# Kernel optimization log

Hardware: AMD Instinct MI355X
Metric: run time of the kernel (lower is better)

The kernel has to match this reference:

```python
import jax, jax.numpy as jnp
import numpy as np

N, E, G = 20000, 320000, 128
D, H, C, L = 128, 8, 16, 4  # hidden, heads, per-head dim, layers
F_NODE, F_EDGE, T = 9, 3, 10


def _lin_init(key, fan_in, shape):
    return jax.random.normal(key, shape, dtype=jnp.float32) / np.sqrt(fan_in)


def setup_inputs() -> dict:
    key = jax.random.key(0)
    ks = jax.random.split(key, 24)
    inp = {
        "x": jax.random.normal(ks[0], (N, F_NODE), dtype=jnp.float32),
        "edge_index": jax.random.randint(ks[1], (2, E), 0, N),
        "edge_attr": jax.random.normal(ks[2], (E, F_EDGE), dtype=jnp.float32),
        "batch": jnp.sort(jax.random.randint(ks[3], (N,), 0, G)),
        # encoders
        "node_w": _lin_init(ks[4], F_NODE, (F_NODE, D)), "node_b": jnp.zeros((D,), jnp.float32),
        "edge_w": _lin_init(ks[5], F_EDGE, (F_EDGE, D)), "edge_b": jnp.zeros((D,), jnp.float32),
        # per-layer TransformerConv params (stacked over L)
        "Wq": _lin_init(ks[6], D, (L, D, D)), "bq": jnp.zeros((L, D), jnp.float32),
        "Wk": _lin_init(ks[7], D, (L, D, D)), "bk": jnp.zeros((L, D), jnp.float32),
        "Wv": _lin_init(ks[8], D, (L, D, D)), "bv": jnp.zeros((L, D), jnp.float32),
        "We": _lin_init(ks[9], D, (L, D, D)),  # lin_edge (no bias in PyG)
        "Wskip": _lin_init(ks[10], D, (L, D, D)), "bskip": jnp.zeros((L, D), jnp.float32),
        "Wbeta": _lin_init(ks[11], 3 * D, (L, 3 * D)),  # lin_beta (no bias)
        "ln_g": jnp.ones((L, D), jnp.float32), "ln_b": jnp.zeros((L, D), jnp.float32),
        # prediction head
        "h1_w": _lin_init(ks[12], D, (D, D // 2)), "h1_b": jnp.zeros((D // 2,), jnp.float32),
        "h2_w": _lin_init(ks[13], D // 2, (D // 2, T)), "h2_b": jnp.zeros((T,), jnp.float32),
    }
    return inp


def _layer_norm(x, g, b, eps=1e-5):
    mu = jnp.mean(x, -1, keepdims=True)
    var = jnp.mean(jnp.square(x - mu), -1, keepdims=True)
    return (x - mu) * jax.lax.rsqrt(var + eps) * g + b


def _transformer_conv(h, ea, src, dst, Wq, bq, Wk, bk, Wv, bv, We, Wskip, bskip, Wbeta):
    # PyG TransformerConv, concat=True, beta=True, edge_dim=D, eval mode (no dropout)
    q = (h @ Wq + bq)[dst].reshape(E, H, C)           # query at destination i
    k = (h @ Wk + bk)[src].reshape(E, H, C)
    v = (h @ Wv + bv)[src].reshape(E, H, C)
    e = (ea @ We).reshape(E, H, C)
    k = k + e
    alpha = jnp.sum(q * k, -1) / np.sqrt(C)           # [E, H]
    m = jax.ops.segment_max(alpha, dst, num_segments=N)
    alpha = jnp.exp(alpha - m[dst])
    denom = jax.ops.segment_sum(alpha, dst, num_segments=N)
    alpha = alpha / (denom[dst] + 1e-16)
    msg = (v + e) * alpha[..., None]                  # [E, H, C]
    out = jax.ops.segment_sum(msg, dst, num_segments=N).reshape(N, D)
    x_r = h @ Wskip + bskip                           # root/skip transform
    beta = jax.nn.sigmoid(jnp.concatenate([out, x_r, out - x_r], -1) @ Wbeta)  # [N]
    return beta[:, None] * x_r + (1.0 - beta)[:, None] * out


def reference(x, edge_index, edge_attr, batch, node_w, node_b, edge_w, edge_b,
              Wq, bq, Wk, bk, Wv, bv, We, Wskip, bskip, Wbeta, ln_g, ln_b,
              h1_w, h1_b, h2_w, h2_b):
    src, dst = edge_index[0], edge_index[1]
    h = jax.nn.relu(x @ node_w + node_b)              # node encoder + relu
    ea = edge_attr @ edge_w + edge_b                  # edge encoder
    for l in range(L):
        h_res = h
        h = _transformer_conv(h, ea, src, dst, Wq[l], bq[l], Wk[l], bk[l],
                              Wv[l], bv[l], We[l], Wskip[l], bskip[l], Wbeta[l])
        h = _layer_norm(h + h_res, ln_g[l], ln_b[l])
    # global mean pool over graphs
    sums = jax.ops.segment_sum(h, batch, num_segments=G)
    cnt = jax.ops.segment_sum(jnp.ones((N,), h.dtype), batch, num_segments=G)
    pooled = sums / jnp.maximum(cnt, 1.0)[:, None]    # [G, D]
    return jax.nn.relu(pooled @ h1_w + h1_b) @ h2_w + h2_b  # [G, T]
```

## Files before the change

kernel.cpp:

```cpp
#include <hip/hip_runtime.h>
#include <hip/hip_bf16.h>

typedef __hip_bfloat16 bf16;
typedef __attribute__((ext_vector_type(8))) short short8;
typedef __attribute__((ext_vector_type(4))) float f32x4;

#define DEV __device__ __forceinline__

DEV float blo(unsigned u) { return __uint_as_float(u << 16); }
DEV float bhi(unsigned u) { return __uint_as_float(u & 0xffff0000u); }

DEV float waveReduceSum(float v) {
#pragma unroll
    for (int m = 1; m < 64; m <<= 1) v += __shfl_xor(v, m);
    return v;
}

DEV float red8(float v) {
    v += __shfl_xor(v, 8);
    v += __shfl_xor(v, 16);
    v += __shfl_xor(v, 32);
    return v;
}

__global__ __launch_bounds__(256) void pack_w_k(
    const float* __restrict__ Wq, const float* __restrict__ Wk,
    const float* __restrict__ Wv, const float* __restrict__ Ws,
    bf16* __restrict__ outp, int L) {
    int t = blockIdx.x * 256 + threadIdx.x;
    if (t >= 4 * L * 16384) return;
    int p = t & 16383;
    int ls = t >> 14;
    int l = ls >> 2, s = ls & 3;
    int j = p & 7, ln = (p >> 3) & 63, kb = (p >> 9) & 3, nb = p >> 11;
    int k = kb * 32 + (ln >> 4) * 8 + j;
    int n = nb * 16 + (ln & 15);
    const float* W = (s == 0) ? Wq : (s == 1) ? Wk : (s == 2) ? Wv : Ws;
    outp[t] = __float2bfloat16(W[(size_t)l * 16384 + k * 128 + n]);
}

__global__ __launch_bounds__(256) void pack_b_k(
    const float* __restrict__ bq, const float* __restrict__ bk,
    const float* __restrict__ bv, const float* __restrict__ bs,
    float* __restrict__ outp, int L) {
    int t = blockIdx.x * 256 + threadIdx.x;
    if (t >= 4 * L * 128) return;
    int d = t & 127;
    int ls = t >> 7;
    int l = ls >> 2, s = ls & 3;
    const float* B = (s == 0) ? bq : (s == 1) ? bk : (s == 2) ? bv : bs;
    outp[t] = B[l * 128 + d];
}

__global__ __launch_bounds__(256) void edge_mats_k(
    const float* __restrict__ edge_w, const float* __restrict__ edge_b,
    const float* __restrict__ We, float* __restrict__ Me, int L) {
    int t = blockIdx.x * 256 + threadIdx.x;
    if (t >= L * 4 * 128) return;
    int n = t & 127, j = (t >> 7) & 3, l = t >> 9;
    const float* W = We + (size_t)l * 16384;
    const float* row = (j < 3) ? (edge_w + j * 128) : edge_b;
    float acc = 0.f;
    for (int d = 0; d < 128; ++d) acc += row[d] * W[d * 128 + n];
    Me[t] = acc;
}

__global__ __launch_bounds__(256) void hist_k(const int* __restrict__ ei,
                                              int* __restrict__ deg, int E) {
    int e = blockIdx.x * 256 + threadIdx.x;
    if (e >= E) return;
    atomicAdd(&deg[ei[E + e]], 1);
}

__global__ __launch_bounds__(1024) void scan_k(const int* __restrict__ deg,
                                               int* __restrict__ off,
                                               int* __restrict__ cursor, int N, int E) {
    __shared__ int part[1024];
    int t = threadIdx.x;
    int chunk = (N + 1023) >> 10;
    int lo = t * chunk, hi = min(lo + chunk, N);
    int s = 0;
    for (int i = lo; i < hi; ++i) s += deg[i];
    part[t] = s;
    __syncthreads();
    for (int d = 1; d < 1024; d <<= 1) {
        int v = (t >= d) ? part[t - d] : 0;
        __syncthreads();
        part[t] += v;
        __syncthreads();
    }
    int base = (t == 0) ? 0 : part[t - 1];
    for (int i = lo; i < hi; ++i) {
        off[i] = base;
        cursor[i] = base;
        base += deg[i];
    }
    if (t == 1023) off[N] = E;
}

__global__ __launch_bounds__(256) void fill_k(const int* __restrict__ ei,
                                              const float* __restrict__ eattr,
                                              int* __restrict__ cursor,
                                              int* __restrict__ el_src,
                                              float4* __restrict__ ea4, int E) {
    int e = blockIdx.x * 256 + threadIdx.x;
    if (e >= E) return;
    int dst = ei[E + e];
    int pos = atomicAdd(&cursor[dst], 1);
    el_src[pos] = ei[e];
    ea4[pos] = make_float4(eattr[e * 3], eattr[e * 3 + 1], eattr[e * 3 + 2], 0.f);
}

__global__ __launch_bounds__(256) void node_enc_k(
    const float* __restrict__ x, const float* __restrict__ w,
    const float* __restrict__ b, float* __restrict__ h,
    bf16* __restrict__ h_bf, int N) {
    int t = blockIdx.x * 256 + threadIdx.x;
    if (t >= N * 128) return;
    int n = t >> 7, d = t & 127;
    float acc = b[d];
#pragma unroll
    for (int i = 0; i < 9; ++i) acc += x[n * 9 + i] * w[i * 128 + d];
    float r = fmaxf(acc, 0.f);
    h[t] = r;
    h_bf[t] = __float2bfloat16(r);
}

__global__ __launch_bounds__(256) void qkvs_k(
    const bf16* __restrict__ A, const bf16* __restrict__ Wp,
    const float* __restrict__ bp,
    bf16* __restrict__ Q, bf16* __restrict__ kv,
    float* __restrict__ S, int M) {
    int tid = threadIdx.x;
    int l = tid & 63, w = tid >> 6;
    int row0 = blockIdx.x * 64;
    const short* Ab = (const short*)A + (size_t)(row0 + (l & 15)) * 128 + ((l >> 4) * 8);
    short8 a[4][4];
#pragma unroll
    for (int mb = 0; mb < 4; ++mb)
#pragma unroll
        for (int kb = 0; kb < 4; ++kb)
            a[mb][kb] = *(const short8*)(Ab + mb * 16 * 128 + kb * 32);
    int colb = w * 32 + (l & 15);
#pragma unroll
    for (int s = 0; s < 4; ++s) {
        const short* Wb = (const short*)Wp + s * 16384;
        short8 bfr[2][4];
#pragma unroll
        for (int nbi = 0; nbi < 2; ++nbi)
#pragma unroll
            for (int kb = 0; kb < 4; ++kb)
                bfr[nbi][kb] = *(const short8*)(Wb + (size_t)(((w * 2 + nbi) * 4 + kb) * 64 + l) * 8);
        f32x4 acc[4][2] = {};
#pragma unroll
        for (int kb = 0; kb < 4; ++kb)
#pragma unroll
            for (int mb = 0; mb < 4; ++mb)
#pragma unroll
                for (int nbi = 0; nbi < 2; ++nbi)
                    acc[mb][nbi] = __builtin_amdgcn_mfma_f32_16x16x32_bf16(
                        a[mb][kb], bfr[nbi][kb], acc[mb][nbi], 0, 0, 0);
        float bias0 = bp[s * 128 + colb];
        float bias1 = bp[s * 128 + colb + 16];
#pragma unroll
        for (int mb = 0; mb < 4; ++mb) {
            int rbase = row0 + mb * 16 + (l >> 4) * 4;
#pragma unroll
            for (int j = 0; j < 4; ++j) {
                int r = rbase + j;
                if (r >= M) continue;
#pragma unroll
                for (int nbi = 0; nbi < 2; ++nbi) {
                    int c = colb + nbi * 16;
                    float v = acc[mb][nbi][j] + (nbi ? bias1 : bias0);
                    if (s == 0) {
                        Q[(size_t)r * 128 + c] = __float2bfloat16(v);
                    } else if (s == 3) {
                        S[(size_t)r * 128 + c] = v;
                    } else {
                        size_t idx = (size_t)r * 256 + (size_t)(c >> 4) * 32 + (c & 15)
                                   + ((s == 2) ? 16 : 0);
                        kv[idx] = __float2bfloat16(v);
                    }
                }
            }
        }
    }
}

__global__ __launch_bounds__(256) void qm_k(
    const bf16* __restrict__ Q, const float* __restrict__ Me,
    float4* __restrict__ qm, int N) {
    int t = blockIdx.x * 256 + threadIdx.x;
    if (t >= N * 8) return;
    int n = t >> 3, hh = t & 7;
    const unsigned* qr = (const unsigned*)Q + (size_t)n * 64 + hh * 8;
    unsigned qq[8];
    *(uint4*)&qq[0] = *(const uint4*)qr;
    *(uint4*)&qq[4] = *(const uint4*)(qr + 4);
    float a0 = 0.f, a1 = 0.f, a2 = 0.f, a3 = 0.f;
#pragma unroll
    for (int k = 0; k < 8; ++k) {
        float x0 = blo(qq[k]), x1 = bhi(qq[k]);
        int d = hh * 16 + 2 * k;
        a0 += x0 * Me[d]       + x1 * Me[d + 1];
        a1 += x0 * Me[128 + d] + x1 * Me[128 + d + 1];
        a2 += x0 * Me[256 + d] + x1 * Me[256 + d + 1];
        a3 += x0 * Me[384 + d] + x1 * Me[384 + d + 1];
    }
    qm[t] = make_float4(a0, a1, a2, a3);
}

__global__ __launch_bounds__(256) void attn_k(
    const int* __restrict__ off, const int* __restrict__ el_src,
    const float4* __restrict__ ea4, const float* __restrict__ Me,
    const float4* __restrict__ qm, const bf16* __restrict__ Q,
    const bf16* __restrict__ kv, const float* __restrict__ S,
    float* __restrict__ h, bf16* __restrict__ h_bf,
    const float* __restrict__ Wb, const float* __restrict__ lng,
    const float* __restrict__ lnb, int N) {
    int gw = (blockIdx.x * 256 + threadIdx.x) >> 6;
    int l = threadIdx.x & 63;
    int nw = (gridDim.x * 256) >> 6;
    int hh = l & 7, sl = l >> 3;
    int d0 = hh * 16 + sl * 2, d1 = d0 + 1;
    float me00 = Me[d0],       me01 = Me[d1];
    float me10 = Me[128 + d0], me11 = Me[128 + d1];
    float me20 = Me[256 + d0], me21 = Me[256 + d1];
    float me30 = Me[384 + d0], me31 = Me[384 + d1];
    float wba0 = Wb[d0],       wba1 = Wb[d1];
    float wbb0 = Wb[128 + d0], wbb1 = Wb[128 + d1];
    float wbc0 = Wb[256 + d0], wbc1 = Wb[256 + d1];
    float g0 = lng[d0], g1 = lng[d1];
    float bb0 = lnb[d0], bb1 = lnb[d1];
    for (int n = gw; n < N; n += nw) {
        const unsigned* qr = (const unsigned*)Q + (size_t)n * 64 + hh * 8;
        unsigned qq[8];
        *(uint4*)&qq[0] = *(const uint4*)qr;
        *(uint4*)&qq[4] = *(const uint4*)(qr + 4);
        float q[16];
#pragma unroll
        for (int k = 0; k < 8; ++k) { q[2 * k] = blo(qq[k]); q[2 * k + 1] = bhi(qq[k]); }
        float4 qmv = qm[(size_t)n * 8 + hh];
        float acc[16] = {};
        float S0 = 0.f, S1 = 0.f, S2 = 0.f, den = 0.f;
        int i0 = off[n], i1 = off[n + 1];
        int nit = (i1 - i0 + 7) >> 3;
        for (int it = 0; it < nit; ++it) {
            int idx = i0 + it * 8 + sl;
            bool ok = idx < i1;
            int ci = ok ? idx : i0;
            int src = el_src[ci];
            float4 ae = ea4[ci];
            const unsigned* kr = (const unsigned*)kv + (size_t)src * 128 + hh * 16;
            unsigned kk[8], vv[8];
            *(uint4*)&kk[0] = *(const uint4*)kr;
            *(uint4*)&kk[4] = *(const uint4*)(kr + 4);
            *(uint4*)&vv[0] = *(const uint4*)(kr + 8);
            *(uint4*)&vv[4] = *(const uint4*)(kr + 12);
            float sd = fmaf(ae.x, qmv.x, fmaf(ae.y, qmv.y, fmaf(ae.z, qmv.z, qmv.w)));
#pragma unroll
            for (int k = 0; k < 8; ++k)
                sd = fmaf(q[2 * k], blo(kk[k]), fmaf(q[2 * k + 1], bhi(kk[k]), sd));
            float p = ok ? __expf(sd * 0.25f) : 0.f;
            den += p;
            S0 = fmaf(p, ae.x, S0);
            S1 = fmaf(p, ae.y, S1);
            S2 = fmaf(p, ae.z, S2);
#pragma unroll
            for (int k = 0; k < 8; ++k) {
                acc[2 * k]     = fmaf(p, blo(vv[k]), acc[2 * k]);
                acc[2 * k + 1] = fmaf(p, bhi(vv[k]), acc[2 * k + 1]);
            }
        }
        den = red8(den); S0 = red8(S0); S1 = red8(S1); S2 = red8(S2);
#pragma unroll
        for (int k = 0; k < 16; ++k) acc[k] = red8(acc[k]);
        float inv = den > 0.f ? 1.f / den : 0.f;
        float o0 = (acc[sl * 2]     + S0 * me00 + S1 * me10 + S2 * me20 + den * me30) * inv;
        float o1 = (acc[sl * 2 + 1] + S0 * me01 + S1 * me11 + S2 * me21 + den * me31) * inv;
        size_t base = (size_t)n * 128;
        float s0 = S[base + d0], s1 = S[base + d1];
        float part = o0 * wba0 + s0 * wbb0 + (o0 - s0) * wbc0
                   + o1 * wba1 + s1 * wbb1 + (o1 - s1) * wbc1;
        float g = waveReduceSum(part);
        float beta = 1.f / (1.f + __expf(-g));
        float y0 = beta * s0 + (1.f - beta) * o0;
        float y1 = beta * s1 + (1.f - beta) * o1;
        float z0 = y0 + h[base + d0];
        float z1 = y1 + h[base + d1];
        float mean = waveReduceSum(z0 + z1) * (1.f / 128.f);
        float c0 = z0 - mean, c1 = z1 - mean;
        float var = waveReduceSum(c0 * c0 + c1 * c1) * (1.f / 128.f);
        float invs = rsqrtf(var + 1e-5f);
        float r0 = c0 * invs * g0 + bb0;
        float r1 = c1 * invs * g1 + bb1;
        h[base + d0] = r0;
        h[base + d1] = r1;
        h_bf[base + d0] = __float2bfloat16(r0);
        h_bf[base + d1] = __float2bfloat16(r1);
    }
}

__global__ __launch_bounds__(256) void pool_partial_k(
    const float* __restrict__ h, const int* __restrict__ batch,
    float* __restrict__ psum, int N) {
    int d = threadIdx.x & 127;
    int half = threadIdx.x >> 7;
    int n0 = blockIdx.x * 64;
    int n1 = min(n0 + 64, N);
    float acc = 0.f;
    int curg = -1;
    for (int n = n0 + half; n < n1; n += 2) {
        int g = batch[n];
        if (g != curg) {
            if (curg >= 0) atomicAdd(&psum[curg * 128 + d], acc);
            acc = 0.f;
            curg = g;
        }
        acc += h[(size_t)n * 128 + d];
    }
    if (curg >= 0) atomicAdd(&psum[curg * 128 + d], acc);
}

__global__ __launch_bounds__(128) void head2_k(
    const float* __restrict__ psum, const int* __restrict__ batch,
    const float* __restrict__ h1w, const float* __restrict__ h1b,
    const float* __restrict__ h2w, const float* __restrict__ h2b,
    float* __restrict__ out, int N) {
    int g = blockIdx.x;
    int t = threadIdx.x;
    auto lb = [&](int val) {
        int lo = 0, hi = N;
        while (lo < hi) {
            int mid = (lo + hi) >> 1;
            if (batch[mid] < val) lo = mid + 1; else hi = mid;
        }
        return lo;
    };
    int s = lb(g), e = lb(g + 1);
    float cnt = fmaxf((float)(e - s), 1.f);
    __shared__ float pl[128];
    __shared__ float hid[64];
    pl[t] = psum[g * 128 + t] / cnt;
    __syncthreads();
    if (t < 64) {
        float a = h1b[t];
        for (int k = 0; k < 128; ++k) a += pl[k] * h1w[k * 64 + t];
        hid[t] = fmaxf(a, 0.f);
    }
    __syncthreads();
    if (t < 10) {
        float o = h2b[t];
        for (int k = 0; k < 64; ++k) o += hid[k] * h2w[k * 10 + t];
        out[g * 10 + t] = o;
    }
}

extern "C" void kernel_launch(void* const* d_in, const int* in_sizes, int n_in,
                              void* d_out, int out_size, void* d_ws, size_t ws_size,
                              hipStream_t stream) {
    const float* x      = (const float*)d_in[0];
    const int*   ei     = (const int*)d_in[1];
    const float* eattr  = (const float*)d_in[2];
    const int*   batch  = (const int*)d_in[3];
    const float* node_w = (const float*)d_in[4];
    const float* node_b = (const float*)d_in[5];
    const float* edge_w = (const float*)d_in[6];
    const float* edge_b = (const float*)d_in[7];
    const float* Wq     = (const float*)d_in[8];
    const float* bq     = (const float*)d_in[9];
    const float* Wk     = (const float*)d_in[10];
    const float* bk     = (const float*)d_in[11];
    const float* Wv     = (const float*)d_in[12];
    const float* bv     = (const float*)d_in[13];
    const float* We     = (const float*)d_in[14];
    const float* Wskip  = (const float*)d_in[15];
    const float* bskip  = (const float*)d_in[16];
    const float* Wbeta  = (const float*)d_in[17];
    const float* ln_g   = (const float*)d_in[18];
    const float* ln_b   = (const float*)d_in[19];
    const float* h1_w   = (const float*)d_in[20];
    const float* h1_b   = (const float*)d_in[21];
    const float* h2_w   = (const float*)d_in[22];
    const float* h2_b   = (const float*)d_in[23];
    float* out = (float*)d_out;

    const int N = in_sizes[3];
    const int E = in_sizes[2] / 3;
    const int L = in_sizes[8] / 16384;
    const int G = out_size / 10;

    char* wptr = (char*)d_ws;
    auto alloc = [&](size_t bytes) {
        char* p = wptr;
        wptr += (bytes + 255) & ~(size_t)255;
        return p;
    };
    float* h      = (float*)alloc((size_t)(N + 64) * 128 * 4);
    bf16*  h_bf   = (bf16*)alloc((size_t)(N + 64) * 128 * 2);
    bf16*  Qb     = (bf16*)alloc((size_t)(N + 64) * 128 * 2);
    bf16*  kv     = (bf16*)alloc((size_t)(N + 64) * 256 * 2);
    float* S      = (float*)alloc((size_t)(N + 64) * 128 * 4);
    float4* qm    = (float4*)alloc((size_t)N * 8 * 16);
    float4* ea4   = (float4*)alloc((size_t)E * 16);
    bf16*  Wpack  = (bf16*)alloc((size_t)4 * L * 16384 * 2);
    float* bpack  = (float*)alloc((size_t)4 * L * 128 * 4);
    float* Me     = (float*)alloc((size_t)L * 4 * 128 * 4);
    int*   deg    = (int*)alloc((size_t)N * 4);
    int*   off    = (int*)alloc((size_t)(N + 1) * 4);
    int*   cursor = (int*)alloc((size_t)N * 4);
    int*   el_src = (int*)alloc((size_t)E * 4);
    float* psum   = (float*)alloc((size_t)G * 128 * 4);

    dim3 b256(256), b128(128);

    pack_w_k<<<(4 * L * 16384 + 255) / 256, b256, 0, stream>>>(Wq, Wk, Wv, Wskip, Wpack, L);
    pack_b_k<<<(4 * L * 128 + 255) / 256, b256, 0, stream>>>(bq, bk, bv, bskip, bpack, L);
    edge_mats_k<<<(L * 4 * 128 + 255) / 256, b256, 0, stream>>>(edge_w, edge_b, We, Me, L);
    hipMemsetAsync(deg, 0, (size_t)N * 4, stream);
    hist_k<<<(E + 255) / 256, b256, 0, stream>>>(ei, deg, E);
    scan_k<<<1, 1024, 0, stream>>>(deg, off, cursor, N, E);
    fill_k<<<(E + 255) / 256, b256, 0, stream>>>(ei, eattr, cursor, el_src, ea4, E);
    node_enc_k<<<(N * 128 + 255) / 256, b256, 0, stream>>>(x, node_w, node_b, h, h_bf, N);

    int gN = (N + 63) / 64;
    int gAttn = (N + 3) / 4;
    int gQm = (N * 8 + 255) / 256;
    for (int l = 0; l < L; ++l) {
        const float* Me_l = Me + (size_t)l * 512;
        qkvs_k<<<gN, b256, 0, stream>>>(h_bf, Wpack + (size_t)l * 4 * 16384,
                                        bpack + (size_t)l * 4 * 128, Qb, kv, S, N);
        qm_k<<<gQm, b256, 0, stream>>>(Qb, Me_l, qm, N);
        attn_k<<<gAttn, b256, 0, stream>>>(off, el_src, ea4, Me_l, qm,
                                           Qb, kv, S, h, h_bf,
                                           Wbeta + (size_t)l * 384,
                                           ln_g + (size_t)l * 128, ln_b + (size_t)l * 128, N);
    }

    hipMemsetAsync(psum, 0, (size_t)G * 128 * 4, stream);
    pool_partial_k<<<gN, b256, 0, stream>>>(h, batch, psum, N);
    head2_k<<<G, b128, 0, stream>>>(psum, batch, h1_w, h1_b, h2_w, h2_b, out, N);
}
```

Measured before the change: 385.0 us.

## Process each node with a two-wave block, splitting edges across waves

The attention kernel now gives each node its own 128-thread block of two waves instead of one wave per node. Each wave handles half of the node's incoming edges, 16 edges per iteration across the block. Per-head partial sums are combined through shared memory. The beta gate and layer-norm reductions now need block-level syncs, with each thread owning one output dimension. This halves the serial edge-loop length per node (~16 edges on average) to expose more memory parallelism, at the cost of extra __syncthreads, shared-memory traffic, and more, shorter blocks.

```diff
diff --git a/kernel.cpp b/kernel.cpp
--- a/kernel.cpp
+++ b/kernel.cpp
@@ -211,7 +211,7 @@
     qm[t] = make_float4(a0, a1, a2, a3);
 }
 
-__global__ __launch_bounds__(256) void attn_k(
+__global__ __launch_bounds__(128) void attn_k(
     const int* __restrict__ off, const int* __restrict__ el_src,
     const float4* __restrict__ ea4, const float* __restrict__ Me,
     const float4* __restrict__ qm, const bf16* __restrict__ Q,
@@ -219,87 +219,102 @@
     float* __restrict__ h, bf16* __restrict__ h_bf,
     const float* __restrict__ Wb, const float* __restrict__ lng,
     const float* __restrict__ lnb, int N) {
-    int gw = (blockIdx.x * 256 + threadIdx.x) >> 6;
-    int l = threadIdx.x & 63;
-    int nw = (gridDim.x * 256) >> 6;
-    int hh = l & 7, sl = l >> 3;
-    int d0 = hh * 16 + sl * 2, d1 = d0 + 1;
-    float me00 = Me[d0],       me01 = Me[d1];
-    float me10 = Me[128 + d0], me11 = Me[128 + d1];
-    float me20 = Me[256 + d0], me21 = Me[256 + d1];
-    float me30 = Me[384 + d0], me31 = Me[384 + d1];
-    float wba0 = Wb[d0],       wba1 = Wb[d1];
-    float wbb0 = Wb[128 + d0], wbb1 = Wb[128 + d1];
-    float wbc0 = Wb[256 + d0], wbc1 = Wb[256 + d1];
-    float g0 = lng[d0], g1 = lng[d1];
-    float bb0 = lnb[d0], bb1 = lnb[d1];
-    for (int n = gw; n < N; n += nw) {
-        const unsigned* qr = (const unsigned*)Q + (size_t)n * 64 + hh * 8;
-        unsigned qq[8];
-        *(uint4*)&qq[0] = *(const uint4*)qr;
-        *(uint4*)&qq[4] = *(const uint4*)(qr + 4);
-        float q[16];
-#pragma unroll
-        for (int k = 0; k < 8; ++k) { q[2 * k] = blo(qq[k]); q[2 * k + 1] = bhi(qq[k]); }
-        float4 qmv = qm[(size_t)n * 8 + hh];
-        float acc[16] = {};
-        float S0 = 0.f, S1 = 0.f, S2 = 0.f, den = 0.f;
-        int i0 = off[n], i1 = off[n + 1];
-        int nit = (i1 - i0 + 7) >> 3;
-        for (int it = 0; it < nit; ++it) {
-            int idx = i0 + it * 8 + sl;
-            bool ok = idx < i1;
-            int ci = ok ? idx : i0;
-            int src = el_src[ci];
-            float4 ae = ea4[ci];
-            const unsigned* kr = (const unsigned*)kv + (size_t)src * 128 + hh * 16;
-            unsigned kk[8], vv[8];
-            *(uint4*)&kk[0] = *(const uint4*)kr;
-            *(uint4*)&kk[4] = *(const uint4*)(kr + 4);
-            *(uint4*)&vv[0] = *(const uint4*)(kr + 8);
-            *(uint4*)&vv[4] = *(const uint4*)(kr + 12);
-            float sd = fmaf(ae.x, qmv.x, fmaf(ae.y, qmv.y, fmaf(ae.z, qmv.z, qmv.w)));
-#pragma unroll
-            for (int k = 0; k < 8; ++k)
-                sd = fmaf(q[2 * k], blo(kk[k]), fmaf(q[2 * k + 1], bhi(kk[k]), sd));
-            float p = ok ? __expf(sd * 0.25f) : 0.f;
-            den += p;
-            S0 = fmaf(p, ae.x, S0);
-            S1 = fmaf(p, ae.y, S1);
-            S2 = fmaf(p, ae.z, S2);
-#pragma unroll
-            for (int k = 0; k < 8; ++k) {
-                acc[2 * k]     = fmaf(p, blo(vv[k]), acc[2 * k]);
-                acc[2 * k + 1] = fmaf(p, bhi(vv[k]), acc[2 * k + 1]);
-            }
+    int n = blockIdx.x;
+    if (n >= N) return;
+    int t = threadIdx.x;
+    int l = t & 63;
+    int wi = t >> 6;
+    int hh = l & 7;
+    int slw = (l >> 3) & 7;
+    int sl = wi * 8 + slw;
+    int d = hh * 16 + sl;
+
+    __shared__ float cl[2][8][20];
+    __shared__ float rA[2], rB[2], rC[2];
+
+    const unsigned* qr = (const unsigned*)Q + (size_t)n * 64 + hh * 8;
+    unsigned qq[8];
+    *(uint4*)&qq[0] = *(const uint4*)qr;
+    *(uint4*)&qq[4] = *(const uint4*)(qr + 4);
+    float q[16];
+#pragma unroll
+    for (int k = 0; k < 8; ++k) { q[2 * k] = blo(qq[k]); q[2 * k + 1] = bhi(qq[k]); }
+    float4 qmv = qm[(size_t)n * 8 + hh];
+
+    float acc[16] = {};
+    float S0 = 0.f, S1 = 0.f, S2 = 0.f, den = 0.f;
+    int i0 = off[n], i1 = off[n + 1];
+    int nit = (i1 - i0 + 15) >> 4;
+    for (int it = 0; it < nit; ++it) {
+        int idx = i0 + it * 16 + sl;
+        bool ok = idx < i1;
+        int ci = ok ? idx : i0;
+        int src = el_src[ci];
+        float4 ae = ea4[ci];
+        const unsigned* kr = (const unsigned*)kv + (size_t)src * 128 + hh * 16;
+        unsigned kk[8], vv[8];
+        *(uint4*)&kk[0] = *(const uint4*)kr;
+        *(uint4*)&kk[4] = *(const uint4*)(kr + 4);
+        *(uint4*)&vv[0] = *(const uint4*)(kr + 8);
+        *(uint4*)&vv[4] = *(const uint4*)(kr + 12);
+        float sd = fmaf(ae.x, qmv.x, fmaf(ae.y, qmv.y, fmaf(ae.z, qmv.z, qmv.w)));
+#pragma unroll
+        for (int k = 0; k < 8; ++k)
+            sd = fmaf(q[2 * k], blo(kk[k]), fmaf(q[2 * k + 1], bhi(kk[k]), sd));
+        float p = ok ? __expf(sd * 0.25f) : 0.f;
+        den += p;
+        S0 = fmaf(p, ae.x, S0);
+        S1 = fmaf(p, ae.y, S1);
+        S2 = fmaf(p, ae.z, S2);
+#pragma unroll
+        for (int k = 0; k < 8; ++k) {
+            acc[2 * k]     = fmaf(p, blo(vv[k]), acc[2 * k]);
+            acc[2 * k + 1] = fmaf(p, bhi(vv[k]), acc[2 * k + 1]);
         }
-        den = red8(den); S0 = red8(S0); S1 = red8(S1); S2 = red8(S2);
-#pragma unroll
-        for (int k = 0; k < 16; ++k) acc[k] = red8(acc[k]);
-        float inv = den > 0.f ? 1.f / den : 0.f;
-        float o0 = (acc[sl * 2]     + S0 * me00 + S1 * me10 + S2 * me20 + den * me30) * inv;
-        float o1 = (acc[sl * 2 + 1] + S0 * me01 + S1 * me11 + S2 * me21 + den * me31) * inv;
-        size_t base = (size_t)n * 128;
-        float s0 = S[base + d0], s1 = S[base + d1];
-        float part = o0 * wba0 + s0 * wbb0 + (o0 - s0) * wbc0
-                   + o1 * wba1 + s1 * wbb1 + (o1 - s1) * wbc1;
-        float g = waveReduceSum(part);
-        float beta = 1.f / (1.f + __expf(-g));
-        float y0 = beta * s0 + (1.f - beta) * o0;
-        float y1 = beta * s1 + (1.f - beta) * o1;
-        float z0 = y0 + h[base + d0];
-        float z1 = y1 + h[base + d1];
-        float mean = waveReduceSum(z0 + z1) * (1.f / 128.f);
-        float c0 = z0 - mean, c1 = z1 - mean;
-        float var = waveReduceSum(c0 * c0 + c1 * c1) * (1.f / 128.f);
-        float invs = rsqrtf(var + 1e-5f);
-        float r0 = c0 * invs * g0 + bb0;
-        float r1 = c1 * invs * g1 + bb1;
-        h[base + d0] = r0;
-        h[base + d1] = r1;
-        h_bf[base + d0] = __float2bfloat16(r0);
-        h_bf[base + d1] = __float2bfloat16(r1);
-    }
+    }
+    den = red8(den); S0 = red8(S0); S1 = red8(S1); S2 = red8(S2);
+#pragma unroll
+    for (int k = 0; k < 16; ++k) acc[k] = red8(acc[k]);
+    if (slw == 0) {
+#pragma unroll
+        for (int k = 0; k < 16; ++k) cl[wi][hh][k] = acc[k];
+        cl[wi][hh][16] = den;
+        cl[wi][hh][17] = S0;
+        cl[wi][hh][18] = S1;
+        cl[wi][hh][19] = S2;
+    }
+    __syncthreads();
+    float accv = cl[0][hh][sl] + cl[1][hh][sl];
+    float denf = cl[0][hh][16] + cl[1][hh][16];
+    float S0f  = cl[0][hh][17] + cl[1][hh][17];
+    float S1f  = cl[0][hh][18] + cl[1][hh][18];
+    float S2f  = cl[0][hh][19] + cl[1][hh][19];
+    float inv = denf > 0.f ? 1.f / denf : 0.f;
+    float o = (accv + S0f * Me[d] + S1f * Me[128 + d] + S2f * Me[256 + d]
+             + denf * Me[384 + d]) * inv;
+    size_t base = (size_t)n * 128;
+    float s = S[base + d];
+    float part = o * Wb[d] + s * Wb[128 + d] + (o - s) * Wb[256 + d];
+    float pw = waveReduceSum(part);
+    if (l == 0) rA[wi] = pw;
+    __syncthreads();
+    float g = rA[0] + rA[1];
+    float beta = 1.f / (1.f + __expf(-g));
+    float y = beta * s + (1.f - beta) * o;
+    float z = y + h[base + d];
+    float mw = waveReduceSum(z);
+    if (l == 0) rB[wi] = mw;
+    __syncthreads();
+    float mean = (rB[0] + rB[1]) * (1.f / 128.f);
+    float c = z - mean;
+    float vw = waveReduceSum(c * c);
+    if (l == 0) rC[wi] = vw;
+    __syncthreads();
+    float var = (rC[0] + rC[1]) * (1.f / 128.f);
+    float invs = rsqrtf(var + 1e-5f);
+    float r = c * invs * lng[d] + lnb[d];
+    h[base + d] = r;
+    h_bf[base + d] = __float2bfloat16(r);
 }
 
 __global__ __launch_bounds__(256) void pool_partial_k(
@@ -425,17 +440,16 @@
     node_enc_k<<<(N * 128 + 255) / 256, b256, 0, stream>>>(x, node_w, node_b, h, h_bf, N);
 
     int gN = (N + 63) / 64;
-    int gAttn = (N + 3) / 4;
     int gQm = (N * 8 + 255) / 256;
     for (int l = 0; l < L; ++l) {
         const float* Me_l = Me + (size_t)l * 512;
         qkvs_k<<<gN, b256, 0, stream>>>(h_bf, Wpack + (size_t)l * 4 * 16384,
                                         bpack + (size_t)l * 4 * 128, Qb, kv, S, N);
         qm_k<<<gQm, b256, 0, stream>>>(Qb, Me_l, qm, N);
-        attn_k<<<gAttn, b256, 0, stream>>>(off, el_src, ea4, Me_l, qm,
-                                           Qb, kv, S, h, h_bf,
-                                           Wbeta + (size_t)l * 384,
-                                           ln_g + (size_t)l * 128, ln_b + (size_t)l * 128, N);
+        attn_k<<<N, b128, 0, stream>>>(off, el_src, ea4, Me_l, qm,
+                                       Qb, kv, S, h, h_bf,
+                                       Wbeta + (size_t)l * 384,
+                                       ln_g + (size_t)l * 128, ln_b + (size_t)l * 128, N);
     }
 
     hipMemsetAsync(psum, 0, (size_t)G * 128 * 4, stream);
```

Result: slower. 437.6 us (+13.6%).

## Fuse qm projection into attention, pack src into edge record, merge prep kernels

Applied to the files above, without the earlier changes.

Removes the separate qm_k kernel by computing the query-edge-matrix products inside attn_k from the already-loaded q values. It also stores the source index in the unused slot of the per-edge float4 record, dropping the el_src array and one gather per edge. The three weight-prep kernels are merged into one launch, and the deg and psum memsets are combined into one. The intent is fewer launches and less memory traffic, at the cost of redundant qm computation across the 8 lanes sharing a head and extra Me loads per node.

```diff
diff --git a/kernel.cpp b/kernel.cpp
--- a/kernel.cpp
+++ b/kernel.cpp
@@ -23,46 +23,45 @@
     return v;
 }
 
-__global__ __launch_bounds__(256) void pack_w_k(
+__global__ __launch_bounds__(256) void prep_k(
     const float* __restrict__ Wq, const float* __restrict__ Wk,
     const float* __restrict__ Wv, const float* __restrict__ Ws,
-    bf16* __restrict__ outp, int L) {
-    int t = blockIdx.x * 256 + threadIdx.x;
-    if (t >= 4 * L * 16384) return;
-    int p = t & 16383;
-    int ls = t >> 14;
-    int l = ls >> 2, s = ls & 3;
-    int j = p & 7, ln = (p >> 3) & 63, kb = (p >> 9) & 3, nb = p >> 11;
-    int k = kb * 32 + (ln >> 4) * 8 + j;
-    int n = nb * 16 + (ln & 15);
-    const float* W = (s == 0) ? Wq : (s == 1) ? Wk : (s == 2) ? Wv : Ws;
-    outp[t] = __float2bfloat16(W[(size_t)l * 16384 + k * 128 + n]);
-}
-
-__global__ __launch_bounds__(256) void pack_b_k(
     const float* __restrict__ bq, const float* __restrict__ bk,
     const float* __restrict__ bv, const float* __restrict__ bs,
-    float* __restrict__ outp, int L) {
+    const float* __restrict__ edge_w, const float* __restrict__ edge_b,
+    const float* __restrict__ We,
+    bf16* __restrict__ Wpack, float* __restrict__ bpack, float* __restrict__ Me, int L) {
     int t = blockIdx.x * 256 + threadIdx.x;
-    if (t >= 4 * L * 128) return;
-    int d = t & 127;
-    int ls = t >> 7;
-    int l = ls >> 2, s = ls & 3;
-    const float* B = (s == 0) ? bq : (s == 1) ? bk : (s == 2) ? bv : bs;
-    outp[t] = B[l * 128 + d];
-}
-
-__global__ __launch_bounds__(256) void edge_mats_k(
-    const float* __restrict__ edge_w, const float* __restrict__ edge_b,
-    const float* __restrict__ We, float* __restrict__ Me, int L) {
-    int t = blockIdx.x * 256 + threadIdx.x;
-    if (t >= L * 4 * 128) return;
-    int n = t & 127, j = (t >> 7) & 3, l = t >> 9;
-    const float* W = We + (size_t)l * 16384;
-    const float* row = (j < 3) ? (edge_w + j * 128) : edge_b;
-    float acc = 0.f;
-    for (int d = 0; d < 128; ++d) acc += row[d] * W[d * 128 + n];
-    Me[t] = acc;
+    int tA = 4 * L * 16384, tB = 4 * L * 128, tC = L * 4 * 128;
+    if (t < tA) {
+        int p = t & 16383;
+        int ls = t >> 14;
+        int l = ls >> 2, s = ls & 3;
+        int j = p & 7, ln = (p >> 3) & 63, kb = (p >> 9) & 3, nb = p >> 11;
+        int k = kb * 32 + (ln >> 4) * 8 + j;
+        int n = nb * 16 + (ln & 15);
+        const float* W = (s == 0) ? Wq : (s == 1) ? Wk : (s == 2) ? Wv : Ws;
+        Wpack[t] = __float2bfloat16(W[(size_t)l * 16384 + k * 128 + n]);
+        return;
+    }
+    t -= tA;
+    if (t < tB) {
+        int d = t & 127;
+        int ls = t >> 7;
+        int l = ls >> 2, s = ls & 3;
+        const float* B = (s == 0) ? bq : (s == 1) ? bk : (s == 2) ? bv : bs;
+        bpack[t] = B[l * 128 + d];
+        return;
+    }
+    t -= tB;
+    if (t < tC) {
+        int n = t & 127, j = (t >> 7) & 3, l = t >> 9;
+        const float* W = We + (size_t)l * 16384;
+        const float* row = (j < 3) ? (edge_w + j * 128) : edge_b;
+        float acc = 0.f;
+        for (int d = 0; d < 128; ++d) acc += row[d] * W[d * 128 + n];
+        Me[t] = acc;
+    }
 }
 
 __global__ __launch_bounds__(256) void hist_k(const int* __restrict__ ei,
@@ -101,14 +100,13 @@
 __global__ __launch_bounds__(256) void fill_k(const int* __restrict__ ei,
                                               const float* __restrict__ eattr,
                                               int* __restrict__ cursor,
-                                              int* __restrict__ el_src,
                                               float4* __restrict__ ea4, int E) {
     int e = blockIdx.x * 256 + threadIdx.x;
     if (e >= E) return;
     int dst = ei[E + e];
     int pos = atomicAdd(&cursor[dst], 1);
-    el_src[pos] = ei[e];
-    ea4[pos] = make_float4(eattr[e * 3], eattr[e * 3 + 1], eattr[e * 3 + 2], 0.f);
+    ea4[pos] = make_float4(__int_as_float(ei[e]),
+                           eattr[e * 3], eattr[e * 3 + 1], eattr[e * 3 + 2]);
 }
 
 __global__ __launch_bounds__(256) void node_enc_k(
@@ -188,33 +186,9 @@
     }
 }
 
-__global__ __launch_bounds__(256) void qm_k(
-    const bf16* __restrict__ Q, const float* __restrict__ Me,
-    float4* __restrict__ qm, int N) {
-    int t = blockIdx.x * 256 + threadIdx.x;
-    if (t >= N * 8) return;
-    int n = t >> 3, hh = t & 7;
-    const unsigned* qr = (const unsigned*)Q + (size_t)n * 64 + hh * 8;
-    unsigned qq[8];
-    *(uint4*)&qq[0] = *(const uint4*)qr;
-    *(uint4*)&qq[4] = *(const uint4*)(qr + 4);
-    float a0 = 0.f, a1 = 0.f, a2 = 0.f, a3 = 0.f;
-#pragma unroll
-    for (int k = 0; k < 8; ++k) {
-        float x0 = blo(qq[k]), x1 = bhi(qq[k]);
-        int d = hh * 16 + 2 * k;
-        a0 += x0 * Me[d]       + x1 * Me[d + 1];
-        a1 += x0 * Me[128 + d] + x1 * Me[128 + d + 1];
-        a2 += x0 * Me[256 + d] + x1 * Me[256 + d + 1];
-        a3 += x0 * Me[384 + d] + x1 * Me[384 + d + 1];
-    }
-    qm[t] = make_float4(a0, a1, a2, a3);
-}
-
 __global__ __launch_bounds__(256) void attn_k(
-    const int* __restrict__ off, const int* __restrict__ el_src,
-    const float4* __restrict__ ea4, const float* __restrict__ Me,
-    const float4* __restrict__ qm, const bf16* __restrict__ Q,
+    const int* __restrict__ off, const float4* __restrict__ ea4,
+    const float* __restrict__ Me, const bf16* __restrict__ Q,
     const bf16* __restrict__ kv, const float* __restrict__ S,
     float* __restrict__ h, bf16* __restrict__ h_bf,
     const float* __restrict__ Wb, const float* __restrict__ lng,
@@ -241,7 +215,18 @@
         float q[16];
 #pragma unroll
         for (int k = 0; k < 8; ++k) { q[2 * k] = blo(qq[k]); q[2 * k + 1] = bhi(qq[k]); }
-        float4 qmv = qm[(size_t)n * 8 + hh];
+        float qm0 = 0.f, qm1 = 0.f, qm2 = 0.f, qm3 = 0.f;
+#pragma unroll
+        for (int c = 0; c < 4; ++c) {
+            float4 r0 = *(const float4*)(Me + hh * 16 + c * 4);
+            float4 r1 = *(const float4*)(Me + 128 + hh * 16 + c * 4);
+            float4 r2 = *(const float4*)(Me + 256 + hh * 16 + c * 4);
+            float4 r3 = *(const float4*)(Me + 384 + hh * 16 + c * 4);
+            qm0 += q[c*4]*r0.x + q[c*4+1]*r0.y + q[c*4+2]*r0.z + q[c*4+3]*r0.w;
+            qm1 += q[c*4]*r1.x + q[c*4+1]*r1.y + q[c*4+2]*r1.z + q[c*4+3]*r1.w;
+            qm2 += q[c*4]*r2.x + q[c*4+1]*r2.y + q[c*4+2]*r2.z + q[c*4+3]*r2.w;
+            qm3 += q[c*4]*r3.x + q[c*4+1]*r3.y + q[c*4+2]*r3.z + q[c*4+3]*r3.w;
+        }
         float acc[16] = {};
         float S0 = 0.f, S1 = 0.f, S2 = 0.f, den = 0.f;
         int i0 = off[n], i1 = off[n + 1];
@@ -250,23 +235,23 @@
             int idx = i0 + it * 8 + sl;
             bool ok = idx < i1;
             int ci = ok ? idx : i0;
-            int src = el_src[ci];
-            float4 ae = ea4[ci];
+            float4 rec = ea4[ci];
+            int src = __float_as_int(rec.x);
             const unsigned* kr = (const unsigned*)kv + (size_t)src * 128 + hh * 16;
             unsigned kk[8], vv[8];
             *(uint4*)&kk[0] = *(const uint4*)kr;
             *(uint4*)&kk[4] = *(const uint4*)(kr + 4);
             *(uint4*)&vv[0] = *(const uint4*)(kr + 8);
             *(uint4*)&vv[4] = *(const uint4*)(kr + 12);
-            float sd = fmaf(ae.x, qmv.x, fmaf(ae.y, qmv.y, fmaf(ae.z, qmv.z, qmv.w)));
+            float sd = fmaf(rec.y, qm0, fmaf(rec.z, qm1, fmaf(rec.w, qm2, qm3)));
 #pragma unroll
             for (int k = 0; k < 8; ++k)
                 sd = fmaf(q[2 * k], blo(kk[k]), fmaf(q[2 * k + 1], bhi(kk[k]), sd));
             float p = ok ? __expf(sd * 0.25f) : 0.f;
             den += p;
-            S0 = fmaf(p, ae.x, S0);
-            S1 = fmaf(p, ae.y, S1);
-            S2 = fmaf(p, ae.z, S2);
+            S0 = fmaf(p, rec.y, S0);
+            S1 = fmaf(p, rec.z, S1);
+            S2 = fmaf(p, rec.w, S2);
 #pragma unroll
             for (int k = 0; k < 8; ++k) {
                 acc[2 * k]     = fmaf(p, blo(vv[k]), acc[2 * k]);
@@ -402,43 +387,40 @@
     bf16*  Qb     = (bf16*)alloc((size_t)(N + 64) * 128 * 2);
     bf16*  kv     = (bf16*)alloc((size_t)(N + 64) * 256 * 2);
     float* S      = (float*)alloc((size_t)(N + 64) * 128 * 4);
-    float4* qm    = (float4*)alloc((size_t)N * 8 * 16);
     float4* ea4   = (float4*)alloc((size_t)E * 16);
     bf16*  Wpack  = (bf16*)alloc((size_t)4 * L * 16384 * 2);
     float* bpack  = (float*)alloc((size_t)4 * L * 128 * 4);
     float* Me     = (float*)alloc((size_t)L * 4 * 128 * 4);
-    int*   deg    = (int*)alloc((size_t)N * 4);
+    size_t degBytes = ((size_t)N * 4 + 255) & ~(size_t)255;
+    char*  zblock = (char*)alloc(degBytes + (size_t)G * 128 * 4);
+    int*   deg    = (int*)zblock;
+    float* psum   = (float*)(zblock + degBytes);
     int*   off    = (int*)alloc((size_t)(N + 1) * 4);
     int*   cursor = (int*)alloc((size_t)N * 4);
-    int*   el_src = (int*)alloc((size_t)E * 4);
-    float* psum   = (float*)alloc((size_t)G * 128 * 4);
 
     dim3 b256(256), b128(128);
 
-    pack_w_k<<<(4 * L * 16384 + 255) / 256, b256, 0, stream>>>(Wq, Wk, Wv, Wskip, Wpack, L);
-    pack_b_k<<<(4 * L * 128 + 255) / 256, b256, 0, stream>>>(bq, bk, bv, bskip, bpack, L);
-    edge_mats_k<<<(L * 4 * 128 + 255) / 256, b256, 0, stream>>>(edge_w, edge_b, We, Me, L);
-    hipMemsetAsync(deg, 0, (size_t)N * 4, stream);
+    int prepTot = 4 * L * 16384 + 4 * L * 128 + L * 4 * 128;
+    prep_k<<<(prepTot + 255) / 256, b256, 0, stream>>>(
+        Wq, Wk, Wv, Wskip, bq, bk, bv, bskip, edge_w, edge_b, We,
+        Wpack, bpack, Me, L);
+    hipMemsetAsync(zblock, 0, degBytes + (size_t)G * 128 * 4, stream);
     hist_k<<<(E + 255) / 256, b256, 0, stream>>>(ei, deg, E);
     scan_k<<<1, 1024, 0, stream>>>(deg, off, cursor, N, E);
-    fill_k<<<(E + 255) / 256, b256, 0, stream>>>(ei, eattr, cursor, el_src, ea4, E);
+    fill_k<<<(E + 255) / 256, b256, 0, stream>>>(ei, eattr, cursor, ea4, E);
     node_enc_k<<<(N * 128 + 255) / 256, b256, 0, stream>>>(x, node_w, node_b, h, h_bf, N);
 
     int gN = (N + 63) / 64;
     int gAttn = (N + 3) / 4;
-    int gQm = (N * 8 + 255) / 256;
     for (int l = 0; l < L; ++l) {
         const float* Me_l = Me + (size_t)l * 512;
         qkvs_k<<<gN, b256, 0, stream>>>(h_bf, Wpack + (size_t)l * 4 * 16384,
                                         bpack + (size_t)l * 4 * 128, Qb, kv, S, N);
-        qm_k<<<gQm, b256, 0, stream>>>(Qb, Me_l, qm, N);
-        attn_k<<<gAttn, b256, 0, stream>>>(off, el_src, ea4, Me_l, qm,
-                                           Qb, kv, S, h, h_bf,
+        attn_k<<<gAttn, b256, 0, stream>>>(off, ea4, Me_l, Qb, kv, S, h, h_bf,
                                            Wbeta + (size_t)l * 384,
                                            ln_g + (size_t)l * 128, ln_b + (size_t)l * 128, N);
     }
 
-    hipMemsetAsync(psum, 0, (size_t)G * 128 * 4, stream);
     pool_partial_k<<<gN, b256, 0, stream>>>(h, batch, psum, N);
     head2_k<<<G, b128, 0, stream>>>(psum, batch, h1_w, h1_b, h2_w, h2_b, out, N);
 }
```

Result: slower. 440.3 us (+14.4%).
